# Kernel optimization log

Hardware: AMD Instinct MI355X
Metric: run time of the kernel (lower is better)

## Reference

```python
import jax, jax.numpy as jnp
import numpy as np

H = 8
D_MODEL = 1024
DIM_G = 64
WAVE_LEN = 1000.0


def box_relational_embedding(f_g):
    # f_g: [B, N, 4] -> [B, N, N, 64] trigonometric geometry embedding
    B, N, _ = f_g.shape
    x_min, y_min, x_max, y_max = jnp.split(f_g, 4, axis=-1)  # each [B, N, 1]
    cx = (x_min + x_max) * 0.5
    cy = (y_min + y_max) * 0.5
    w = x_max - x_min + 1.0
    h = y_max - y_min + 1.0
    # row i vs column j deltas, normalized by row box size
    dx = jnp.log(jnp.maximum(jnp.abs((cx - cx.reshape(B, 1, N)) / w), 1e-3))
    dy = jnp.log(jnp.maximum(jnp.abs((cy - cy.reshape(B, 1, N)) / h), 1e-3))
    dw = jnp.log(w / w.reshape(B, 1, N))
    dh = jnp.log(h / h.reshape(B, 1, N))
    pos = jnp.stack([dx, dy, dw, dh], axis=-1)  # [B, N, N, 4]
    feat_range = jnp.arange(DIM_G // 8, dtype=jnp.float32) / (DIM_G / 8.0)
    dim_mat = 1.0 / jnp.power(WAVE_LEN, feat_range)  # [8]
    mul = (100.0 * pos)[..., None] * dim_mat  # [B, N, N, 4, 8]
    mul = mul.reshape(B, N, N, DIM_G // 2)
    return jnp.concatenate([jnp.sin(mul), jnp.cos(mul)], axis=-1)  # [B, N, N, 64]


def setup_inputs() -> dict:
    key = jax.random.key(0)
    ks = jax.random.split(key, 12)
    B, N, D = 16, 256, D_MODEL
    q = jax.random.normal(ks[0], (B, N, D), jnp.float32)
    k = jax.random.normal(ks[1], (B, N, D), jnp.float32)
    v = jax.random.normal(ks[2], (B, N, D), jnp.float32)
    # valid boxes: x_max > x_min, y_max > y_min
    xy = jax.random.uniform(ks[3], (B, N, 2), jnp.float32) * 100.0
    wh = jax.random.uniform(ks[4], (B, N, 2), jnp.float32) * 50.0 + 1.0
    input_box = jnp.concatenate([xy, xy + wh], axis=-1)  # [B, N, 4]
    s = 0.02
    Wq = jax.random.normal(ks[5], (D, D), jnp.float32) * s
    Wk = jax.random.normal(ks[6], (D, D), jnp.float32) * s
    Wv = jax.random.normal(ks[7], (D, D), jnp.float32) * s
    Wo = jax.random.normal(ks[8], (D, D), jnp.float32) * s
    bq = jnp.zeros((D,), jnp.float32)
    bk = jnp.zeros((D,), jnp.float32)
    bv = jnp.zeros((D,), jnp.float32)
    bo = jnp.zeros((D,), jnp.float32)
    Wg = jax.random.normal(ks[9], (H, DIM_G), jnp.float32) * 0.1  # stacked per-head Linear(64,1)
    bg = jax.random.normal(ks[10], (H,), jnp.float32) * 0.1
    return {"input_query": q, "input_key": k, "input_value": v, "input_box": input_box,
            "Wq": Wq, "bq": bq, "Wk": Wk, "bk": bk, "Wv": Wv, "bv": bv,
            "Wg": Wg, "bg": bg, "Wo": Wo, "bo": bo}


def reference(input_query, input_key, input_value, input_box,
              Wq, bq, Wk, bk, Wv, bv, Wg, bg, Wo, bo):
    B, N, D = input_query.shape
    d_k = D // H

    def proj(x, W, b):
        return (x @ W + b).reshape(B, N, H, d_k).transpose(0, 2, 1, 3)  # [B,H,N,dk]

    q = proj(input_query, Wq, bq)
    k = proj(input_key, Wk, bk)
    v = proj(input_value, Wv, bv)

    emb = box_relational_embedding(input_box)  # [B, N, N, 64]
    # per-head Linear(64 -> 1), stacked: [B, H, N, N]
    rel_w = jax.nn.relu(jnp.einsum('bmng,hg->bhmn', emb, Wg) + bg[None, :, None, None])

    scores = jnp.einsum('bhqd,bhkd->bhqk', q, k) / np.sqrt(d_k).astype(np.float32)
    logits = jnp.log(jnp.maximum(rel_w, 1e-6)) + scores
    attn = jax.nn.softmax(logits, axis=-1)  # [B, H, N, N]
    out = jnp.einsum('bhqk,bhkd->bhqd', attn, v)
    out = out.transpose(0, 2, 1, 3).reshape(B, N, D)
    return out @ Wo + bo
```

## Files before the change

kernel.cpp:

```cpp
#include <hip/hip_runtime.h>
#include <hip/hip_bf16.h>
#include <hip/hip_fp16.h>
#include <math.h>

#define B_  16
#define N_  256
#define D_  1024
#define H_  8
#define DK_ 128

typedef unsigned short u16;
typedef __attribute__((ext_vector_type(8))) short s8v;
typedef __attribute__((ext_vector_type(4))) float f4v;

__device__ __forceinline__ u16 f2b(float x) {
    union { float f; unsigned u; } v; v.f = x;
    unsigned r = v.u + 0x7fffu + ((v.u >> 16) & 1u);
    return (u16)(r >> 16);
}

__device__ __forceinline__ void gload16(void* lds, const void* g) {
    __builtin_amdgcn_global_load_lds(
        (const __attribute__((address_space(1))) void*)g,
        (__attribute__((address_space(3))) void*)lds, 16, 0, 0);
}

__device__ __forceinline__ void waitv8() { asm volatile("s_waitcnt vmcnt(8)" ::: "memory"); }
__device__ __forceinline__ void waitv6() { asm volatile("s_waitcnt vmcnt(6)" ::: "memory"); }
__device__ __forceinline__ void waitv4() { asm volatile("s_waitcnt vmcnt(4)" ::: "memory"); }
__device__ __forceinline__ void waitv3() { asm volatile("s_waitcnt vmcnt(3)" ::: "memory"); }
__device__ __forceinline__ void waitv0() { asm volatile("s_waitcnt vmcnt(0)" ::: "memory"); }
__device__ __forceinline__ void membar() { asm volatile("" ::: "memory"); }

__global__ __launch_bounds__(256)
void cvt_kernel(const float* __restrict__ x0, const float* __restrict__ x1,
                const float* __restrict__ x2, u16* __restrict__ out)
{
    const float* in = (blockIdx.y == 0) ? x0 : (blockIdx.y == 1) ? x1 : x2;
    u16* o = out + (size_t)blockIdx.y * 4194304;
    const int i = blockIdx.x * 256 + threadIdx.x;
    const float4 a = ((const float4*)in)[2 * i];
    const float4 b = ((const float4*)in)[2 * i + 1];
    union { u16 s[8]; uint4 v; } t;
    t.s[0] = f2b(a.x); t.s[1] = f2b(a.y); t.s[2] = f2b(a.z); t.s[3] = f2b(a.w);
    t.s[4] = f2b(b.x); t.s[5] = f2b(b.y); t.s[6] = f2b(b.z); t.s[7] = f2b(b.w);
    ((uint4*)o)[i] = t.v;
}

__global__ __launch_bounds__(256)
void cvtT_kernel(const float* __restrict__ W0, const float* __restrict__ W1,
                 const float* __restrict__ W2, const float* __restrict__ W3,
                 u16* __restrict__ out)
{
    const float* W = (blockIdx.z == 0) ? W0 : (blockIdx.z == 1) ? W1 :
                     (blockIdx.z == 2) ? W2 : W3;
    u16* o = out + (size_t)blockIdx.z * (D_ * D_);
    __shared__ float t[32][33];
    const int k0 = blockIdx.x * 32, n0 = blockIdx.y * 32;
    const int c = threadIdx.x & 31, r8 = threadIdx.x >> 5;
#pragma unroll
    for (int rr = 0; rr < 4; ++rr)
        t[r8 + rr * 8][c] = W[(size_t)(k0 + r8 + rr * 8) * D_ + n0 + c];
    __syncthreads();
#pragma unroll
    for (int rr = 0; rr < 4; ++rr)
        o[(size_t)(n0 + r8 + rr * 8) * D_ + k0 + c] = f2b(t[c][r8 + rr * 8]);
}

template<int BM, int FM, int LOADS, int MODE>
__global__ __launch_bounds__(256)
void gemm_kernel(const u16* __restrict__ A0, const u16* __restrict__ Wt0,
                 const float* __restrict__ b0, const float* __restrict__ b1,
                 const float* __restrict__ b2, void* __restrict__ outb)
{
    constexpr int WM  = FM * 16;
    constexpr int MT8 = (4096 / BM) / 8;
    __shared__ __align__(16) u16 As[3][BM][32];
    __shared__ __align__(16) u16 Bs[3][128][32];

    const int z = blockIdx.z;
    const u16* A  = A0  + (size_t)z * 4194304;
    const u16* Wt = Wt0 + (size_t)z * 1048576;
    const float* bias = (z == 0) ? b0 : (z == 1) ? b1 : b2;

    const int bid = blockIdx.x;
    const int xcd = bid & 7;
    const int wic = bid >> 3;
    const int by  = xcd * MT8 + (wic & (MT8 - 1));
    const int bx  = wic / MT8;
    const int m0  = by * BM;
    const int n0  = bx * 128;

    const int tid  = threadIdx.x;
    const int lane = tid & 63;
    const int w    = tid >> 6;
    const int l15  = lane & 15;
    const int l4   = lane >> 4;
    const int wr   = w >> 1;
    const int wc   = w & 1;

    const int gr   = tid >> 2;
    const int c4   = tid & 3;
    const int scol = (c4 ^ ((gr >> 1) & 3)) * 8;
    const int doff = c4 * 8;
    const u16* asrc = A  + (size_t)(m0 + gr) * 1024 + scol;
    const u16* bsrc = Wt + (size_t)(n0 + gr) * 1024 + scol;
    const int fc = (l4 ^ ((l15 >> 1) & 3)) * 8;

    auto stage = [&](int buf, int kt) {
        const int k0_ = kt * 32;
        gload16(&As[buf][gr][doff], asrc + k0_);
        if constexpr (BM == 128)
            gload16(&As[buf][gr + 64][doff], asrc + 64 * 1024 + k0_);
        gload16(&Bs[buf][gr][doff], bsrc + k0_);
        gload16(&Bs[buf][gr + 64][doff], bsrc + 64 * 1024 + k0_);
    };

    f4v acc[FM][4] = {};

    stage(0, 0);
    stage(1, 1);
    int cur = 0, stg = 2;

    for (int kt = 0; kt < 32; ++kt) {
        membar();
        __builtin_amdgcn_s_barrier();
        if (kt < 30) {
            stage(stg, kt + 2);
            if constexpr (LOADS == 4) waitv8(); else waitv6();
        } else if (kt == 30) {
            if constexpr (LOADS == 4) waitv4(); else waitv3();
        } else {
            waitv0();
        }
        membar();
        __builtin_amdgcn_s_barrier();

        s8v af[FM], bf[4];
#pragma unroll
        for (int i = 0; i < FM; ++i)
            af[i] = *(const s8v*)&As[cur][wr * WM + i * 16 + l15][fc];
#pragma unroll
        for (int j = 0; j < 4; ++j)
            bf[j] = *(const s8v*)&Bs[cur][wc * 64 + j * 16 + l15][fc];
#pragma unroll
        for (int i = 0; i < FM; ++i)
#pragma unroll
            for (int j = 0; j < 4; ++j)
                acc[i][j] = __builtin_amdgcn_mfma_f32_16x16x32_bf16(
                    af[i], bf[j], acc[i][j], 0, 0, 0);

        cur = (cur == 2) ? 0 : cur + 1;
        stg = (stg == 2) ? 0 : stg + 1;
    }

#pragma unroll
    for (int j = 0; j < 4; ++j) {
        const int n = n0 + wc * 64 + j * 16 + l15;
        const float bb = bias[n];
#pragma unroll
        for (int i = 0; i < FM; ++i) {
            const int mbase = m0 + wr * WM + i * 16 + l4 * 4;
            if constexpr (MODE == 0) {
#pragma unroll
                for (int reg = 0; reg < 4; ++reg)
                    ((float*)outb)[(size_t)(mbase + reg) * 1024 + n] =
                        acc[i][j][reg] + bb;
            } else {
                if (z == 2) {
                    const int b = mbase >> 8, tok = mbase & 255;
                    const int h = n >> 7, d = n & 127;
                    ushort4 st;
                    st.x = f2b(acc[i][j][0] + bb);
                    st.y = f2b(acc[i][j][1] + bb);
                    st.z = f2b(acc[i][j][2] + bb);
                    st.w = f2b(acc[i][j][3] + bb);
                    *(ushort4*)&((u16*)outb)[(size_t)z * 4194304 +
                        (((size_t)b * H_ + h) * DK_ + d) * N_ + tok] = st;
                } else {
                    const int h = n >> 7, d = n & 127;
#pragma unroll
                    for (int reg = 0; reg < 4; ++reg) {
                        const int m = mbase + reg;
                        const int b = m >> 8, tok = m & 255;
                        ((u16*)outb)[(size_t)z * 4194304 +
                            (((size_t)b * H_ + h) * N_ + tok) * DK_ + d] =
                            f2b(acc[i][j][reg] + bb);
                    }
                }
            }
        }
    }
}

__global__ __launch_bounds__(256)
void boxbias_kernel(const float* __restrict__ fg, const float* __restrict__ Wg,
                    const float* __restrict__ bg, _Float16* __restrict__ lb)
{
    __shared__ __align__(16) float sWg[512];
    __shared__ float sbg[8];
    const int tid = threadIdx.x;
    const int b = blockIdx.x >> 8;
    const int i = blockIdx.x & 255;

    sWg[tid] = Wg[tid];
    sWg[tid + 256] = Wg[tid + 256];
    if (tid < 8) sbg[tid] = bg[tid];

    const float4 bi = *(const float4*)&fg[(size_t)(b * N_ + i) * 4];
    const float cxi = 0.5f * (bi.x + bi.z);
    const float cyi = 0.5f * (bi.y + bi.w);
    const float wi  = bi.z - bi.x + 1.0f;
    const float hi  = bi.w - bi.y + 1.0f;

    const int j = tid;
    const float4 bj = *(const float4*)&fg[(size_t)(b * N_ + j) * 4];
    const float cxj = 0.5f * (bj.x + bj.z);
    const float cyj = 0.5f * (bj.y + bj.w);
    const float wj  = bj.z - bj.x + 1.0f;
    const float hj  = bj.w - bj.y + 1.0f;

    const float pos[4] = {
        logf(fmaxf(fabsf((cxi - cxj) / wi), 1e-3f)) * 100.0f,
        logf(fmaxf(fabsf((cyi - cyj) / hi), 1e-3f)) * 100.0f,
        logf(wi / wj) * 100.0f,
        logf(hi / hj) * 100.0f
    };
    const float dim[8] = {1.0f, 0.421696503f, 0.177827941f, 0.0749894209f,
                          0.0316227766f, 0.0133352143f, 0.00562341325f, 0.00237137371f};

    float sv[32], cv[32];
#pragma unroll
    for (int p = 0; p < 4; ++p)
#pragma unroll
        for (int q = 0; q < 8; ++q)
            __sincosf(pos[p] * dim[q], &sv[p * 8 + q], &cv[p * 8 + q]);

    __syncthreads();
#pragma unroll
    for (int h = 0; h < 8; ++h) {
        float acc = sbg[h];
        const float* wrow = &sWg[h * 64];
#pragma unroll
        for (int g0 = 0; g0 < 32; g0 += 4) {
            const float4 ws = *(const float4*)&wrow[g0];
            const float4 wc = *(const float4*)&wrow[32 + g0];
            acc = fmaf(sv[g0 + 0], ws.x, fmaf(cv[g0 + 0], wc.x, acc));
            acc = fmaf(sv[g0 + 1], ws.y, fmaf(cv[g0 + 1], wc.y, acc));
            acc = fmaf(sv[g0 + 2], ws.z, fmaf(cv[g0 + 2], wc.z, acc));
            acc = fmaf(sv[g0 + 3], ws.w, fmaf(cv[g0 + 3], wc.w, acc));
        }
        const float rel = fmaxf(acc, 0.0f);
        lb[(((size_t)b * H_ + h) * N_ + i) * N_ + j] =
            (_Float16)logf(fmaxf(rel, 1e-6f));
    }
}

__global__ __launch_bounds__(256)
void attn_mfma_kernel(const u16* __restrict__ qp, const u16* __restrict__ kp,
                      const u16* __restrict__ vp, const _Float16* __restrict__ lb,
                      u16* __restrict__ ao)
{
    __shared__ __align__(16) u16 Ks[32][136];
    __shared__ __align__(16) u16 Vt[128][40];
    __shared__ __align__(16) u16 Ps[4][16][40];

    const int tid  = threadIdx.x;
    const int lane = tid & 63;
    const int w    = tid >> 6;
    const int l15  = lane & 15;
    const int l4   = lane >> 4;
    const int bh   = blockIdx.x >> 2;
    const int qt   = blockIdx.x & 3;
    const int q0   = qt * 64 + w * 16;

    s8v qf[4];
    const u16* qb = qp + ((size_t)bh * N_ + q0) * DK_;
#pragma unroll
    for (int ks = 0; ks < 4; ++ks)
        qf[ks] = *(const s8v*)(qb + (size_t)l15 * DK_ + ks * 32 + l4 * 8);

    f4v o[8] = {};
    float m_r[4], l_r[4];
#pragma unroll
    for (int r = 0; r < 4; ++r) { m_r[r] = -INFINITY; l_r[r] = 0.0f; }

    const float scale = 0.08838834764831845f;
    const _Float16* lbb = lb + ((size_t)bh * N_ + q0) * N_;

    const int sr = tid >> 3;
    const int sc = (tid & 7) * 16;
    const int vr = tid >> 2;
    const int vs = (tid & 3) * 8;

    for (int kt = 0; kt < 8; ++kt) {
        __syncthreads();
        {
            const u16* ksrc = kp + ((size_t)bh * N_ + kt * 32) * DK_;
            *(s8v*)&Ks[sr][sc]     = *(const s8v*)(ksrc + (size_t)sr * DK_ + sc);
            *(s8v*)&Ks[sr][sc + 8] = *(const s8v*)(ksrc + (size_t)sr * DK_ + sc + 8);
        }
        {
            const u16* vsrc = vp + ((size_t)bh * DK_ + vr) * N_ + kt * 32 + vs;
            const s8v v0 = *(const s8v*)vsrc;
            const s8v v1 = *(const s8v*)(vsrc + 64 * N_);
            *(s8v*)&Vt[vr][vs]      = v0;
            *(s8v*)&Vt[vr + 64][vs] = v1;
        }
        __syncthreads();

        f4v s[2] = {};
#pragma unroll
        for (int ks = 0; ks < 4; ++ks) {
#pragma unroll
            for (int kf = 0; kf < 2; ++kf) {
                const s8v kb = *(const s8v*)&Ks[kf * 16 + l15][ks * 32 + l4 * 8];
                s[kf] = __builtin_amdgcn_mfma_f32_16x16x32_bf16(
                    qf[ks], kb, s[kf], 0, 0, 0);
            }
        }
#pragma unroll
        for (int kf = 0; kf < 2; ++kf)
#pragma unroll
            for (int r = 0; r < 4; ++r)
                s[kf][r] = fmaf(s[kf][r], scale, (float)
                    lbb[(size_t)(l4 * 4 + r) * N_ + kt * 32 + kf * 16 + l15]);

        {
            float rm[4], al[4];
#pragma unroll
            for (int r = 0; r < 4; ++r) rm[r] = fmaxf(s[0][r], s[1][r]);
#pragma unroll
            for (int st = 1; st <= 8; st <<= 1)
#pragma unroll
                for (int r = 0; r < 4; ++r) rm[r] = fmaxf(rm[r], __shfl_xor(rm[r], st));
#pragma unroll
            for (int r = 0; r < 4; ++r) {
                const float mn = fmaxf(m_r[r], rm[r]);
                al[r] = __expf(m_r[r] - mn);
                m_r[r] = mn;
            }
            float p0[4], p1[4], rs[4];
#pragma unroll
            for (int r = 0; r < 4; ++r) {
                p0[r] = __expf(s[0][r] - m_r[r]);
                p1[r] = __expf(s[1][r] - m_r[r]);
                rs[r] = p0[r] + p1[r];
            }
#pragma unroll
            for (int st = 1; st <= 8; st <<= 1)
#pragma unroll
                for (int r = 0; r < 4; ++r) rs[r] += __shfl_xor(rs[r], st);
#pragma unroll
            for (int r = 0; r < 4; ++r) {
                l_r[r] = l_r[r] * al[r] + rs[r];
                Ps[w][l4 * 4 + r][l15]      = f2b(p0[r]);
                Ps[w][l4 * 4 + r][16 + l15] = f2b(p1[r]);
            }
#pragma unroll
            for (int nf = 0; nf < 8; ++nf)
#pragma unroll
                for (int r = 0; r < 4; ++r) o[nf][r] *= al[r];
        }

        const s8v pa = *(const s8v*)&Ps[w][l15][l4 * 8];
#pragma unroll
        for (int nf = 0; nf < 8; ++nf) {
            const s8v vb = *(const s8v*)&Vt[nf * 16 + l15][l4 * 8];
            o[nf] = __builtin_amdgcn_mfma_f32_16x16x32_bf16(pa, vb, o[nf], 0, 0, 0);
        }
    }

    const int b = bh >> 3, h = bh & 7;
    float inv[4];
#pragma unroll
    for (int r = 0; r < 4; ++r) inv[r] = 1.0f / l_r[r];
#pragma unroll
    for (int nf = 0; nf < 8; ++nf) {
#pragma unroll
        for (int r = 0; r < 4; ++r) {
            const int tok = q0 + l4 * 4 + r;
            const int d = nf * 16 + l15;
            ao[(((size_t)b * N_ + tok) * H_ + h) * DK_ + d] = f2b(o[nf][r] * inv[r]);
        }
    }
}

extern "C" void kernel_launch(void* const* d_in, const int* in_sizes, int n_in,
                              void* d_out, int out_size, void* d_ws, size_t ws_size,
                              hipStream_t stream)
{
    const float* xq = (const float*)d_in[0];
    const float* xk = (const float*)d_in[1];
    const float* xv = (const float*)d_in[2];
    const float* fg = (const float*)d_in[3];
    const float* Wq = (const float*)d_in[4];
    const float* bq = (const float*)d_in[5];
    const float* Wk = (const float*)d_in[6];
    const float* bk = (const float*)d_in[7];
    const float* Wv = (const float*)d_in[8];
    const float* bv = (const float*)d_in[9];
    const float* Wg = (const float*)d_in[10];
    const float* bg = (const float*)d_in[11];
    const float* Wo = (const float*)d_in[12];
    const float* bo = (const float*)d_in[13];

    char* w8 = (char*)d_ws;
    u16*      xb  = (u16*)(w8);
    u16*      Wt  = (u16*)(w8 + 25165824);
    u16*      qkv = (u16*)(w8 + 33554432);
    _Float16* lb  = (_Float16*)(w8 + 58720256);
    u16*      ao  = (u16*)(w8 + 75497472);

    cvt_kernel<<<dim3(2048, 3), 256, 0, stream>>>(xq, xk, xv, xb);
    cvtT_kernel<<<dim3(32, 32, 4), 256, 0, stream>>>(Wq, Wk, Wv, Wo, Wt);

    gemm_kernel<128, 4, 4, 1><<<dim3(256, 1, 3), 256, 0, stream>>>(
        xb, Wt, bq, bk, bv, qkv);

    boxbias_kernel<<<B_ * N_, 256, 0, stream>>>(fg, Wg, bg, lb);

    attn_mfma_kernel<<<512, 256, 0, stream>>>(
        qkv, qkv + 4194304, qkv + 2 * 4194304, lb, ao);

    gemm_kernel<64, 2, 3, 0><<<dim3(512, 1, 1), 256, 0, stream>>>(
        ao, Wt + 3 * 1048576, bo, bo, bo, d_out);
}
```

Measured before the change: 126.6 us.

## Replace block-tiled GEMM with single-wave 64x64 GEMM without barriers

Both projection GEMMs now use a one-wavefront kernel that computes a 64x64 output tile and does all of its own global-to-LDS staging. This removes the workgroup s_barrier pairs, relying on vmcnt/lgkmcnt waits within the single wave. The grid grows to 1024 blocks per matrix. The trade-off is less data reuse per block, because each wave loads its A and B tiles alone, plus heavier per-wave load issue and more global traffic.

```diff
diff --git a/kernel.cpp b/kernel.cpp
--- a/kernel.cpp
+++ b/kernel.cpp
@@ -25,12 +25,13 @@
         (__attribute__((address_space(3))) void*)lds, 16, 0, 0);
 }
 
-__device__ __forceinline__ void waitv8() { asm volatile("s_waitcnt vmcnt(8)" ::: "memory"); }
-__device__ __forceinline__ void waitv6() { asm volatile("s_waitcnt vmcnt(6)" ::: "memory"); }
-__device__ __forceinline__ void waitv4() { asm volatile("s_waitcnt vmcnt(4)" ::: "memory"); }
-__device__ __forceinline__ void waitv3() { asm volatile("s_waitcnt vmcnt(3)" ::: "memory"); }
-__device__ __forceinline__ void waitv0() { asm volatile("s_waitcnt vmcnt(0)" ::: "memory"); }
-__device__ __forceinline__ void membar() { asm volatile("" ::: "memory"); }
+__device__ __forceinline__ void waitv16() { asm volatile("s_waitcnt vmcnt(16)" ::: "memory"); }
+__device__ __forceinline__ void waitv8()  { asm volatile("s_waitcnt vmcnt(8)"  ::: "memory"); }
+__device__ __forceinline__ void waitv0()  { asm volatile("s_waitcnt vmcnt(0)"  ::: "memory"); }
+__device__ __forceinline__ void waitlgkm0() {
+    asm volatile("s_waitcnt lgkmcnt(0)" ::: "memory");
+    __builtin_amdgcn_sched_barrier(0);
+}
 
 __global__ __launch_bounds__(256)
 void cvt_kernel(const float* __restrict__ x0, const float* __restrict__ x1,
@@ -67,16 +68,14 @@
         o[(size_t)(n0 + r8 + rr * 8) * D_ + k0 + c] = f2b(t[c][r8 + rr * 8]);
 }
 
-template<int BM, int FM, int LOADS, int MODE>
-__global__ __launch_bounds__(256)
-void gemm_kernel(const u16* __restrict__ A0, const u16* __restrict__ Wt0,
-                 const float* __restrict__ b0, const float* __restrict__ b1,
-                 const float* __restrict__ b2, void* __restrict__ outb)
-{
-    constexpr int WM  = FM * 16;
-    constexpr int MT8 = (4096 / BM) / 8;
-    __shared__ __align__(16) u16 As[3][BM][32];
-    __shared__ __align__(16) u16 Bs[3][128][32];
+template<int MODE>
+__global__ __launch_bounds__(64)
+void wgemm_kernel(const u16* __restrict__ A0, const u16* __restrict__ Wt0,
+                  const float* __restrict__ b0, const float* __restrict__ b1,
+                  const float* __restrict__ b2, void* __restrict__ outb)
+{
+    __shared__ __align__(16) u16 As[3][64][32];
+    __shared__ __align__(16) u16 Bs[3][64][32];
 
     const int z = blockIdx.z;
     const u16* A  = A0  + (size_t)z * 4194304;
@@ -86,81 +85,67 @@
     const int bid = blockIdx.x;
     const int xcd = bid & 7;
     const int wic = bid >> 3;
-    const int by  = xcd * MT8 + (wic & (MT8 - 1));
-    const int bx  = wic / MT8;
-    const int m0  = by * BM;
-    const int n0  = bx * 128;
-
-    const int tid  = threadIdx.x;
-    const int lane = tid & 63;
-    const int w    = tid >> 6;
+    const int by  = xcd * 8 + (wic & 7);
+    const int bx  = wic >> 3;
+    const int m0  = by * 64;
+    const int n0  = bx * 64;
+
+    const int lane = threadIdx.x;
     const int l15  = lane & 15;
     const int l4   = lane >> 4;
-    const int wr   = w >> 1;
-    const int wc   = w & 1;
-
-    const int gr   = tid >> 2;
-    const int c4   = tid & 3;
-    const int scol = (c4 ^ ((gr >> 1) & 3)) * 8;
-    const int doff = c4 * 8;
-    const u16* asrc = A  + (size_t)(m0 + gr) * 1024 + scol;
-    const u16* bsrc = Wt + (size_t)(n0 + gr) * 1024 + scol;
+
+    const int srow = lane >> 2;
+    const int sch  = lane & 3;
+    const int scol = (sch ^ ((srow >> 1) & 3)) * 8;
+    const u16* aS = A  + (size_t)(m0 + srow) * 1024 + scol;
+    const u16* bS = Wt + (size_t)(n0 + srow) * 1024 + scol;
     const int fc = (l4 ^ ((l15 >> 1) & 3)) * 8;
 
     auto stage = [&](int buf, int kt) {
         const int k0_ = kt * 32;
-        gload16(&As[buf][gr][doff], asrc + k0_);
-        if constexpr (BM == 128)
-            gload16(&As[buf][gr + 64][doff], asrc + 64 * 1024 + k0_);
-        gload16(&Bs[buf][gr][doff], bsrc + k0_);
-        gload16(&Bs[buf][gr + 64][doff], bsrc + 64 * 1024 + k0_);
+#pragma unroll
+        for (int i = 0; i < 4; ++i)
+            gload16(&As[buf][i * 16 + srow][sch * 8], aS + (size_t)i * 16 * 1024 + k0_);
+#pragma unroll
+        for (int i = 0; i < 4; ++i)
+            gload16(&Bs[buf][i * 16 + srow][sch * 8], bS + (size_t)i * 16 * 1024 + k0_);
     };
 
-    f4v acc[FM][4] = {};
+    f4v acc[4][4] = {};
 
     stage(0, 0);
     stage(1, 1);
-    int cur = 0, stg = 2;
 
     for (int kt = 0; kt < 32; ++kt) {
-        membar();
-        __builtin_amdgcn_s_barrier();
-        if (kt < 30) {
-            stage(stg, kt + 2);
-            if constexpr (LOADS == 4) waitv8(); else waitv6();
-        } else if (kt == 30) {
-            if constexpr (LOADS == 4) waitv4(); else waitv3();
-        } else {
-            waitv0();
-        }
-        membar();
-        __builtin_amdgcn_s_barrier();
-
-        s8v af[FM], bf[4];
-#pragma unroll
-        for (int i = 0; i < FM; ++i)
-            af[i] = *(const s8v*)&As[cur][wr * WM + i * 16 + l15][fc];
+        const int cur = kt % 3;
+        waitlgkm0();
+        if (kt < 30) stage((kt + 2) % 3, kt + 2);
+        if (kt < 30)      waitv16();
+        else if (kt == 30) waitv8();
+        else               waitv0();
+
+        s8v af[4], bf[4];
+#pragma unroll
+        for (int i = 0; i < 4; ++i)
+            af[i] = *(const s8v*)&As[cur][i * 16 + l15][fc];
 #pragma unroll
         for (int j = 0; j < 4; ++j)
-            bf[j] = *(const s8v*)&Bs[cur][wc * 64 + j * 16 + l15][fc];
-#pragma unroll
-        for (int i = 0; i < FM; ++i)
+            bf[j] = *(const s8v*)&Bs[cur][j * 16 + l15][fc];
+#pragma unroll
+        for (int i = 0; i < 4; ++i)
 #pragma unroll
             for (int j = 0; j < 4; ++j)
                 acc[i][j] = __builtin_amdgcn_mfma_f32_16x16x32_bf16(
                     af[i], bf[j], acc[i][j], 0, 0, 0);
-
-        cur = (cur == 2) ? 0 : cur + 1;
-        stg = (stg == 2) ? 0 : stg + 1;
     }
 
 #pragma unroll
     for (int j = 0; j < 4; ++j) {
-        const int n = n0 + wc * 64 + j * 16 + l15;
+        const int n = n0 + j * 16 + l15;
         const float bb = bias[n];
 #pragma unroll
-        for (int i = 0; i < FM; ++i) {
-            const int mbase = m0 + wr * WM + i * 16 + l4 * 4;
+        for (int i = 0; i < 4; ++i) {
+            const int mbase = m0 + i * 16 + l4 * 4;
             if constexpr (MODE == 0) {
 #pragma unroll
                 for (int reg = 0; reg < 4; ++reg)
@@ -415,7 +400,7 @@
     cvt_kernel<<<dim3(2048, 3), 256, 0, stream>>>(xq, xk, xv, xb);
     cvtT_kernel<<<dim3(32, 32, 4), 256, 0, stream>>>(Wq, Wk, Wv, Wo, Wt);
 
-    gemm_kernel<128, 4, 4, 1><<<dim3(256, 1, 3), 256, 0, stream>>>(
+    wgemm_kernel<1><<<dim3(1024, 1, 3), 64, 0, stream>>>(
         xb, Wt, bq, bk, bv, qkv);
 
     boxbias_kernel<<<B_ * N_, 256, 0, stream>>>(fg, Wg, bg, lb);
@@ -423,6 +408,6 @@
     attn_mfma_kernel<<<512, 256, 0, stream>>>(
         qkv, qkv + 4194304, qkv + 2 * 4194304, lb, ao);
 
-    gemm_kernel<64, 2, 3, 0><<<dim3(512, 1, 1), 256, 0, stream>>>(
+    wgemm_kernel<0><<<dim3(1024, 1, 1), 64, 0, stream>>>(
         ao, Wt + 3 * 1048576, bo, bo, bo, d_out);
 }
```

Result: slower. 148.9 us (+17.6%).
